# Kernel tuning notes

Measured on AMD Instinct MI355X. Metric: run time of the kernel, lower is better.

## Reference

```python
import jax, jax.numpy as jnp
import numpy as np

B, C, H, W = 4, 128, 96, 96
E = 4
C8 = C // 8


def _conv1x1(w, b, x):
    # w: [out, in], x: [b, in, H, W]
    return jnp.einsum('oi,bihw->bohw', w, x) + b[None, :, None, None]


def _bilinear_zeros(x, gx, gy):
    # x: [b, C, h, w]; gx, gy: [b, H2, W2] normalized coords in [-1, 1]
    # align_corners=True, padding_mode='zeros' (matches F.grid_sample)
    b, c, h, w = x.shape
    ix = (gx + 1.0) * 0.5 * (w - 1)
    iy = (gy + 1.0) * 0.5 * (h - 1)
    ix0 = jnp.floor(ix)
    iy0 = jnp.floor(iy)
    tx = ix - ix0
    ty = iy - iy0
    ix0 = ix0.astype(jnp.int32)
    iy0 = iy0.astype(jnp.int32)

    def gather(yy, xx):
        valid = ((xx >= 0) & (xx < w) & (yy >= 0) & (yy < h)).astype(x.dtype)
        xc = jnp.clip(xx, 0, w - 1)
        yc = jnp.clip(yy, 0, h - 1)
        vals = jax.vmap(lambda xb, y, xi: xb[:, y, xi])(x, yc, xc)  # [b,C,H2,W2]
        return vals * valid[:, None]

    w00 = ((1 - tx) * (1 - ty))[:, None]
    w01 = (tx * (1 - ty))[:, None]
    w10 = ((1 - tx) * ty)[:, None]
    w11 = (tx * ty)[:, None]
    return (gather(iy0, ix0) * w00 + gather(iy0, ix0 + 1) * w01
            + gather(iy0 + 1, ix0) * w10 + gather(iy0 + 1, ix0 + 1) * w11)


def setup_inputs() -> dict:
    key = jax.random.key(0)
    ks = jax.random.split(key, 12)
    s = 0.05
    return {
        'x': jax.random.normal(ks[0], (B, C, H, W), jnp.float32),
        'weight_compress': jax.random.normal(ks[1], (E, C8, C), jnp.float32) * s,
        'weight_expand': jax.random.normal(ks[2], (E, C, C8), jnp.float32) * s,
        'body_w1': jax.random.normal(ks[3], (64, 3), jnp.float32) * s,
        'body_b1': jax.random.normal(ks[4], (64,), jnp.float32) * s,
        'body_w2': jax.random.normal(ks[5], (64, 64), jnp.float32) * s,
        'body_b2': jax.random.normal(ks[6], (64,), jnp.float32) * s,
        'rout_w': jax.random.normal(ks[7], (E, 64), jnp.float32) * s,
        'rout_b': jax.random.normal(ks[8], (E,), jnp.float32) * s,
        'off_w': jax.random.normal(ks[9], (2, 64), jnp.float32) * s,
        'off_b': jax.random.normal(ks[10], (2,), jnp.float32) * s,
        'scale': 2,
    }


def reference(x, weight_compress, weight_expand, body_w1, body_b1,
              body_w2, body_b2, rout_w, rout_b, off_w, off_b, scale):
    b, c, h, w = x.shape
    sc = float(scale)
    H2 = round(h * sc)
    W2 = round(w * sc)

    # fractional sub-pixel coordinates (meta-upsample positional encoding)
    ch = (jnp.arange(H2, dtype=jnp.float32) + 0.5) / sc
    ch = ch - jnp.floor(ch + 0.001) - 0.5  # [H2]
    cw = (jnp.arange(W2, dtype=jnp.float32) + 0.5) / sc
    cw = cw - jnp.floor(cw + 0.001) - 0.5  # [W2]
    inp = jnp.stack([
        jnp.full((H2, W2), 1.0 / sc, jnp.float32),
        jnp.broadcast_to(ch[:, None], (H2, W2)),
        jnp.broadcast_to(cw[None, :], (H2, W2)),
    ], axis=0)[None]  # [1, 3, H2, W2]

    emb = jax.nn.relu(_conv1x1(body_w1, body_b1, inp))
    emb = jax.nn.relu(_conv1x1(body_w2, body_b2, emb))
    offset = _conv1x1(off_w, off_b, emb)                      # [1, 2, H2, W2]
    routing = jax.nn.sigmoid(_conv1x1(rout_w, rout_b, emb))   # [1, E, H2, W2]
    r = routing[0].transpose(1, 2, 0)                         # [H2, W2, E]

    # base sampling grid, align_corners=True normalization + learned offset
    gx = ((jnp.arange(W2, dtype=jnp.float32) + 0.5) / sc - 0.5) * 2.0 / (w - 1) - 1.0
    gy = ((jnp.arange(H2, dtype=jnp.float32) + 0.5) / sc - 0.5) * 2.0 / (h - 1) - 1.0
    gx = gx[None, None, :] + offset[:, 0] * 2.0 / (w - 1)     # [1, H2, W2]
    gy = gy[None, :, None] + offset[:, 1] * 2.0 / (h - 1)
    gx = jnp.broadcast_to(gx, (b, H2, W2))
    gy = jnp.broadcast_to(gy, (b, H2, W2))

    fea0 = _bilinear_zeros(x, gx, gy)          # [b, C, H2, W2]
    fea = fea0.transpose(0, 2, 3, 1)           # [b, H2, W2, C]

    # per-pixel routed 1x1 convs: compress (C->C/8) then expand (C/8->C)
    comp = jnp.einsum('bhwc,hwe,eoc->bhwo', fea, r, weight_compress)
    out = jnp.einsum('bhwo,hwe,eco->bhwc', comp, r, weight_expand)
    return out.transpose(0, 3, 1, 2) + fea0
```

## Files before the change

### kernel.cpp

```cpp
#include <hip/hip_runtime.h>
#include <math.h>

#define Bn 4
#define Cc 128
#define Hh 96
#define Ww 96
#define H2c 192
#define W2c 192
#define HW (Hh*Ww)
#define HW2 (H2c*W2c)

#define WC_OFF 0
#define WE_OFF (4*2048)
#define TAP_OFF (8*2048)
#define M_OFF  16640

typedef float  f32x4  __attribute__((ext_vector_type(4)));
typedef short  s16x8  __attribute__((ext_vector_type(8)));

__device__ __forceinline__ unsigned f2bf(float f) {
    unsigned u = __float_as_uint(f);
    return (u + 0x7FFFu + ((u >> 16) & 1u)) >> 16;
}

__device__ __forceinline__ void gload_lds16(const float* g, float* l) {
    __builtin_amdgcn_global_load_lds(
        (const __attribute__((address_space(1))) unsigned int*)g,
        (__attribute__((address_space(3))) unsigned int*)l,
        16, 0, 0);
}

__global__ __launch_bounds__(256) void k1_mix(
    const float* __restrict__ wcomp, const float* __restrict__ wexp,
    const float* __restrict__ bw1, const float* __restrict__ bb1,
    const float* __restrict__ bw2, const float* __restrict__ bb2,
    const float* __restrict__ rw,  const float* __restrict__ rb,
    const float* __restrict__ ow,  const float* __restrict__ ob,
    float* __restrict__ ws)
{
    __shared__ float e1[64], e2[64], rr[4], of[2];
    const int tid   = threadIdx.x;
    const int cls   = blockIdx.x >> 4;
    const int chunk = blockIdx.x & 15;
    const float chv = (cls & 2) ? 0.25f : -0.25f;
    const float cwv = (cls & 1) ? 0.25f : -0.25f;

    if (tid < 64) {
        float h = bw1[tid*3+0]*0.5f + bw1[tid*3+1]*chv + bw1[tid*3+2]*cwv + bb1[tid];
        e1[tid] = fmaxf(h, 0.f);
    }
    __syncthreads();
    if (tid < 64) {
        float s = bb2[tid];
        for (int i = 0; i < 64; ++i) s += bw2[tid*64+i]*e1[i];
        e2[tid] = fmaxf(s, 0.f);
    }
    __syncthreads();
    if (tid < 6) {
        if (tid < 4) {
            float s = rb[tid];
            for (int i = 0; i < 64; ++i) s += rw[tid*64+i]*e2[i];
            rr[tid] = 1.f/(1.f+expf(-s));
        } else {
            const int d = tid - 4;
            float s = ob[d];
            for (int i = 0; i < 64; ++i) s += ow[d*64+i]*e2[i];
            of[d] = s;
        }
    }
    __syncthreads();
    const float r0 = rr[0], r1 = rr[1], r2 = rr[2], r3 = rr[3];

    if (tid < 128) {
        const int idx = chunk*128 + tid;
        const int o = idx >> 7, c = idx & 127;
        const float v = r0*wcomp[idx] + r1*wcomp[2048+idx]
                      + r2*wcomp[4096+idx] + r3*wcomp[6144+idx];
        ws[WC_OFF + cls*2048 + c*16 + o] = v;
    } else {
        const int idx = chunk*128 + (tid - 128);
        ws[WE_OFF + cls*2048 + idx] =
            r0*wexp[idx] + r1*wexp[2048+idx] + r2*wexp[4096+idx] + r3*wexp[6144+idx];
    }
    if (chunk == 0 && tid == 0) {
        const float fx = cwv + of[0];
        const float fy = chv + of[1];
        const float Dx = floorf(fx), Dy = floorf(fy);
        ws[TAP_OFF + cls*4 + 0] = fx - Dx;
        ws[TAP_OFF + cls*4 + 1] = fy - Dy;
        ws[TAP_OFF + cls*4 + 2] = Dx;
        ws[TAP_OFF + cls*4 + 3] = Dy;
    }
}

__global__ __launch_bounds__(256) void k1b_fold(
    const float* __restrict__ wsr, unsigned short* __restrict__ Mw)
{
    const int t   = blockIdx.x*256 + threadIdx.x;
    const int cls = t >> 12;
    const int rem = t & 4095;
    const int co  = rem >> 5;
    const int ci0 = (rem & 31) * 4;
    const float* we = wsr + WE_OFF + cls*2048 + co*16;

    float m[4];
    #pragma unroll
    for (int q = 0; q < 4; ++q) {
        const float* wc = wsr + WC_OFF + cls*2048 + (ci0+q)*16;
        float s = 0.f;
        #pragma unroll
        for (int o = 0; o < 16; ++o) s += we[o]*wc[o];
        if (co == ci0 + q) s += 1.f;
        m[q] = s;
    }
    uint2 v;
    v.x = f2bf(m[0]) | (f2bf(m[1]) << 16);
    v.y = f2bf(m[2]) | (f2bf(m[3]) << 16);
    *reinterpret_cast<uint2*>(Mw + (size_t)cls*16384 + co*128 + ci0) = v;
}

__device__ __forceinline__ void remap_axis(int c0, int last, float w0, float w1,
                                           int& base, float& a0, float& a1)
{
    base = min(max(c0, 0), last - 1);
    if (c0 >= 0 && c0 < last) { a0 = w0;  a1 = w1;  }
    else if (c0 == -1)        { a0 = w1;  a1 = 0.f; }
    else if (c0 == last)      { a0 = 0.f; a1 = w0;  }
    else                      { a0 = 0.f; a1 = 0.f; }
}

__global__ __launch_bounds__(256) void k2_mfma(
    const float* __restrict__ x, const float* __restrict__ wsr,
    const unsigned short* __restrict__ Mw, float* __restrict__ out)
{
    __shared__ __align__(16) unsigned short lF[64*128];
    __shared__ __align__(16) float lWin[4*2048];

    const int tid = threadIdx.x;
    const int xl  = tid & 63;
    const int grp = tid >> 6;

    const int n = blockIdx.x;
    const int w = (n & 7)*288 + (n >> 3);
    const int cls  = w & 3;
    const int px_  = cls & 1, py = (cls >> 1) & 1;
    const int rest = w >> 2;
    const int tile = rest % 144;
    const int b    = rest / 144;
    const int jt = tile/3, xs = tile - jt*3;
    const int j0 = jt*2, i0 = xs*32;

    const unsigned short* Mc = Mw + (size_t)cls*16384;
    const int lo = xl & 15, hi = xl >> 4;
    s16x8 a[2][4];
    #pragma unroll
    for (int t = 0; t < 2; ++t)
        #pragma unroll
        for (int kk = 0; kk < 4; ++kk)
            a[t][kk] = *reinterpret_cast<const s16x8*>(
                Mc + (32*grp + 16*t + lo)*128 + kk*32 + hi*8);

    const int pr = xl >> 5, pc = xl & 31;
    const int j = j0 + pr, i = i0 + pc;

    const float tx = wsr[TAP_OFF + cls*4 + 0];
    const float ty = wsr[TAP_OFF + cls*4 + 1];
    const int   Dx = (int)wsr[TAP_OFF + cls*4 + 2];
    const int   Dy = (int)wsr[TAP_OFF + cls*4 + 3];
    int basex, basey; float ax0, ax1, ay0, ay1;
    remap_axis(i + Dx, Ww - 1, 1.f - tx, tx, basex, ax0, ax1);
    remap_axis(j + Dy, Hh - 1, 1.f - ty, ty, basey, ay0, ay1);
    const float w00 = ay0*ax0, w01 = ay0*ax1, w10 = ay1*ax0, w11 = ay1*ax1;

    const int c0  = i0 + Dx;
    const int cs0 = min(max(0, c0 & ~3), Ww - 40);
    const int cidx = basex - cs0;
    const int ro0 = pr*40 + cidx;
    const int ro1 = ro0 + 40;

    const int jD = j0 + Dy;
    const int sl = xl & 31;
    const int s2 = min(sl, 29);
    const int lr = s2 / 10, lq = s2 - lr*10;
    const int lrow = min(max(jD + lr, 0), Hh - 1);
    const float* gsrc = x + (size_t)b*Cc*HW + (size_t)lrow*Ww + cs0 + 4*lq;
    const int chsub = xl >> 5;

    float* winw = lWin + grp*2048;

    #pragma unroll
    for (int h = 0; h < 2; ++h) {
        #pragma unroll
        for (int p = 0; p < 8; ++p) {
            const int ch = grp*32 + h*16 + p*2 + chsub;
            gload_lds16(gsrc + (size_t)ch*HW, winw + p*256);
        }
        asm volatile("s_waitcnt vmcnt(0)" ::: "memory");
        __builtin_amdgcn_sched_barrier(0);
        #pragma unroll
        for (int cq = 0; cq < 4; ++cq) {
            float f[4];
            #pragma unroll
            for (int u = 0; u < 4; ++u) {
                const float* wc = winw + (cq*4 + u)*128;
                f[u] = w00*wc[ro0] + w01*wc[ro0+1] + w10*wc[ro1] + w11*wc[ro1+1];
            }
            uint2 v;
            v.x = f2bf(f[0]) | (f2bf(f[1]) << 16);
            v.y = f2bf(f[2]) | (f2bf(f[3]) << 16);
            const int c = grp*32 + h*16 + cq*4;
            int byte = xl*256 + c*2;
            byte ^= (xl & 7) << 4;
            *reinterpret_cast<uint2*>(reinterpret_cast<char*>(lF) + byte) = v;
        }
        if (h == 0) {
            asm volatile("s_waitcnt lgkmcnt(0)" ::: "memory");
            __builtin_amdgcn_sched_barrier(0);
        }
    }
    __syncthreads();

    f32x4 acc[2][4];
    #pragma unroll
    for (int t = 0; t < 2; ++t)
        #pragma unroll
        for (int nn = 0; nn < 4; ++nn) acc[t][nn] = (f32x4){0.f, 0.f, 0.f, 0.f};

    #pragma unroll
    for (int kk = 0; kk < 4; ++kk) {
        #pragma unroll
        for (int nn = 0; nn < 4; ++nn) {
            int byte = (nn*16 + lo)*256 + kk*64 + hi*16;
            byte ^= (lo & 7) << 4;
            const s16x8 bf = *reinterpret_cast<const s16x8*>(
                reinterpret_cast<const char*>(lF) + byte);
            acc[0][nn] = __builtin_amdgcn_mfma_f32_16x16x32_bf16(a[0][kk], bf, acc[0][nn], 0, 0, 0);
            acc[1][nn] = __builtin_amdgcn_mfma_f32_16x16x32_bf16(a[1][kk], bf, acc[1][nn], 0, 0, 0);
        }
    }

    #pragma unroll
    for (int t = 0; t < 2; ++t)
        #pragma unroll
        for (int nn = 0; nn < 4; ++nn) {
            const int slot2 = nn*16 + lo;
            const int pr2 = slot2 >> 5, pc2 = slot2 & 31;
            const int yg = 2*(j0 + pr2) + py;
            const int xg = 2*(i0 + pc2) + px_;
            const int ch0 = 32*grp + 16*t + hi*4;
            float* op = out + ((size_t)(b*Cc + ch0)*H2c + yg)*W2c + xg;
            #pragma unroll
            for (int r = 0; r < 4; ++r)
                op[(size_t)r*HW2] = acc[t][nn][r];
        }
}

extern "C" void kernel_launch(void* const* d_in, const int* in_sizes, int n_in,
                              void* d_out, int out_size, void* d_ws, size_t ws_size,
                              hipStream_t stream) {
    const float* x     = (const float*)d_in[0];
    const float* wcomp = (const float*)d_in[1];
    const float* wexp  = (const float*)d_in[2];
    const float* bw1   = (const float*)d_in[3];
    const float* bb1   = (const float*)d_in[4];
    const float* bw2   = (const float*)d_in[5];
    const float* bb2   = (const float*)d_in[6];
    const float* rw    = (const float*)d_in[7];
    const float* rb    = (const float*)d_in[8];
    const float* ow    = (const float*)d_in[9];
    const float* ob    = (const float*)d_in[10];
    float* out = (float*)d_out;
    float* ws  = (float*)d_ws;
    unsigned short* Mw = (unsigned short*)(ws + M_OFF);

    k1_mix<<<64, 256, 0, stream>>>(wcomp, wexp, bw1, bb1, bw2, bb2, rw, rb, ow, ob, ws);
    k1b_fold<<<64, 256, 0, stream>>>(ws, Mw);
    k2_mfma<<<2304, 256, 0, stream>>>(x, ws, Mw, out);
}
```

Before: 42.97 us.

## Double-buffer per-wave window loads to overlap global fetch with bilinear compute

Replaces the two-phase load-all-then-compute staging of input window channels with an 8-stage double-buffered pipeline. Each wave issues loads for 4 channels ahead while interpolating the current 4, using partial vmcnt waits. This halves the per-wave LDS window buffer and is meant to hide global load latency behind the bilinear math. It adds more wait points and exposes latency whenever the per-stage compute is too short to cover a load.

Result: slower. 45.60 us (+6.1%).

```diff
diff --git a/kernel.cpp b/kernel.cpp
--- a/kernel.cpp
+++ b/kernel.cpp
@@ -134,7 +134,7 @@
     const unsigned short* __restrict__ Mw, float* __restrict__ out)
 {
     __shared__ __align__(16) unsigned short lF[64*128];
-    __shared__ __align__(16) float lWin[4*2048];
+    __shared__ __align__(16) float lWin[4*2*512];
 
     const int tid = threadIdx.x;
     const int xl  = tid & 63;
@@ -186,38 +186,44 @@
     const float* gsrc = x + (size_t)b*Cc*HW + (size_t)lrow*Ww + cs0 + 4*lq;
     const int chsub = xl >> 5;
 
-    float* winw = lWin + grp*2048;
-
-    #pragma unroll
-    for (int h = 0; h < 2; ++h) {
-        #pragma unroll
-        for (int p = 0; p < 8; ++p) {
-            const int ch = grp*32 + h*16 + p*2 + chsub;
-            gload_lds16(gsrc + (size_t)ch*HW, winw + p*256);
-        }
-        asm volatile("s_waitcnt vmcnt(0)" ::: "memory");
+    float* winw = lWin + grp*1024;
+
+#define ISSUE(q) { \
+    _Pragma("unroll") \
+    for (int p = 0; p < 2; ++p) \
+        gload_lds16(gsrc + (size_t)(grp*32 + (q)*4 + p*2 + chsub)*HW, \
+                    winw + ((q)&1)*512 + p*256); }
+
+    ISSUE(0)
+    ISSUE(1)
+    #pragma unroll
+    for (int q = 0; q < 8; ++q) {
+        if (q < 7) asm volatile("s_waitcnt vmcnt(2)" ::: "memory");
+        else       asm volatile("s_waitcnt vmcnt(0)" ::: "memory");
         __builtin_amdgcn_sched_barrier(0);
-        #pragma unroll
-        for (int cq = 0; cq < 4; ++cq) {
+        {
+            const float* wb = winw + (q&1)*512;
             float f[4];
             #pragma unroll
             for (int u = 0; u < 4; ++u) {
-                const float* wc = winw + (cq*4 + u)*128;
+                const float* wc = wb + (u>>1)*256 + (u&1)*128;
                 f[u] = w00*wc[ro0] + w01*wc[ro0+1] + w10*wc[ro1] + w11*wc[ro1+1];
             }
             uint2 v;
             v.x = f2bf(f[0]) | (f2bf(f[1]) << 16);
             v.y = f2bf(f[2]) | (f2bf(f[3]) << 16);
-            const int c = grp*32 + h*16 + cq*4;
+            const int c = grp*32 + q*4;
             int byte = xl*256 + c*2;
             byte ^= (xl & 7) << 4;
             *reinterpret_cast<uint2*>(reinterpret_cast<char*>(lF) + byte) = v;
         }
-        if (h == 0) {
+        if (q < 6) {
             asm volatile("s_waitcnt lgkmcnt(0)" ::: "memory");
             __builtin_amdgcn_sched_barrier(0);
-        }
-    }
+            ISSUE(q+2)
+        }
+    }
+#undef ISSUE
     __syncthreads();
 
     f32x4 acc[2][4];
```
